# Kernel tuning notes

Hardware: AMD Instinct MI355X
Metric: run time of the kernel (lower is better)

## Reference

```python
import jax, jax.numpy as jnp
import numpy as np

N, L, E, H = 8, 2048, 1024, 1024
EPS = 1e-5


def layernorm(x, g, b):
    m = jnp.mean(x, axis=-1, keepdims=True)
    v = jnp.var(x, axis=-1, keepdims=True)
    return (x - m) * jax.lax.rsqrt(v + EPS) * g + b


def setup_inputs() -> dict:
    key = jax.random.key(0)
    ks = jax.random.split(key, 6)
    s = 0.02
    return {
        "X": jax.random.normal(ks[0], (N, L, E), dtype=jnp.float32),
        "Wq": jax.random.normal(ks[1], (E, H), dtype=jnp.float32) * s,
        "bq": jnp.zeros((H,), jnp.float32),
        "Wk": jax.random.normal(ks[2], (E, H), dtype=jnp.float32) * s,
        "bk": jnp.zeros((H,), jnp.float32),
        "Wv": jax.random.normal(ks[3], (E, H), dtype=jnp.float32) * s,
        "bv": jnp.zeros((H,), jnp.float32),
        "Wf": jax.random.normal(ks[4], (H, H), dtype=jnp.float32) * s,
        "bf": jnp.zeros((H,), jnp.float32),
        "g1": jnp.ones((H,), jnp.float32),
        "b1": jnp.zeros((H,), jnp.float32),
        "g2": jnp.ones((H,), jnp.float32),
        "b2": jnp.zeros((H,), jnp.float32),
    }


def reference(X, Wq, bq, Wk, bk, Wv, bv, Wf, bf, g1, b1, g2, b2):
    scale = 1.0 / jnp.sqrt(jnp.float32(H))
    # both Q and K scaled by 1/sqrt(H) as in source (effective 1/H)
    Q = (X @ Wq + bq) * scale          # (N, L, H)
    K = (X @ Wk + bk) * scale          # (N, L, H)
    V = X @ Wv + bv                    # (N, L, H)
    A = jnp.einsum('nah,nbh->nab', Q, K)   # (N, Lq, Lk)
    A = jax.nn.softmax(A, axis=1)           # softmax over QUERY axis (dim=1), as in source
    # einsum('nll,nlh->nlh') = diagonal of A scaling V elementwise
    diag = jnp.diagonal(A, axis1=1, axis2=2)  # (N, L)
    O = diag[..., None] * V                   # (N, L, H)
    h = layernorm(O + X, g1, b1)
    h = layernorm(h @ Wf + bf + h, g2, b2)
    return h
```

## Files before the change

### kernel.cpp

```cpp
#include <hip/hip_runtime.h>
#include <math.h>

#define NB   8
#define LLEN 2048
#define HDIM 1024
#define LNEPS 1e-5f

#define BM 256
#define BN 256
#define BK 64
#define NT_K (HDIM / BK)
#define NT_K8 (HDIM / 128)
#define NTHR 512
#define SLOT (BM * BK)
#define SLOT8 32768

typedef __attribute__((ext_vector_type(8))) short short8;
typedef __attribute__((ext_vector_type(4))) unsigned short ushort4v;
typedef __attribute__((ext_vector_type(4))) float f32x4;
typedef __attribute__((ext_vector_type(4))) int int4v;
typedef __attribute__((ext_vector_type(8))) int int8v;
typedef __attribute__((ext_vector_type(8))) unsigned char uchar8;

typedef __attribute__((address_space(3))) void lds_void;
typedef const __attribute__((address_space(1))) void glob_void;

__device__ __forceinline__ unsigned short f2bf(float f) {
    union { float f; unsigned u; } v; v.f = f;
    unsigned r = v.u + 0x7FFFu + ((v.u >> 16) & 1u);
    return (unsigned short)(r >> 16);
}
__device__ __forceinline__ float bf2f(unsigned short h) {
    union { unsigned u; float f; } v; v.u = ((unsigned)h) << 16;
    return v.f;
}

__device__ __forceinline__ unsigned char f2fp8(float x) {
    union { float f; unsigned u; } v; v.f = x;
    unsigned s = (v.u >> 24) & 0x80u;
    float a = fabsf(x);
    if (!(a < 448.f)) return (unsigned char)(s | 0x7E);
    int e = (int)((v.u >> 23) & 0xFF) - 127;
    if (e < -6) e = -6;
    float q = rintf(ldexpf(a, 3 - e));
    if (q >= 16.f) { q *= 0.5f; e += 1; }
    int qi = (int)q;
    unsigned byte = (qi < 8) ? (unsigned)qi
                             : (((unsigned)(e + 7) << 3) | (unsigned)(qi - 8));
    return (unsigned char)(s | byte);
}
__device__ __forceinline__ float fp8d(unsigned char b) {
    int e = (b >> 3) & 15, m = b & 7;
    float v = e ? ldexpf((float)(8 + m), e - 10) : ldexpf((float)m, -9);
    return (b & 0x80) ? -v : v;
}

__device__ __forceinline__ unsigned pack4_fp8(float a, float b, float c, float d) {
#if __has_builtin(__builtin_amdgcn_cvt_pk_fp8_f32)
    int r = __builtin_amdgcn_cvt_pk_fp8_f32(a, b, 0, false);
    r = __builtin_amdgcn_cvt_pk_fp8_f32(c, d, r, true);
    return (unsigned)r;
#else
    return (unsigned)f2fp8(a) | ((unsigned)f2fp8(b) << 8)
         | ((unsigned)f2fp8(c) << 16) | ((unsigned)f2fp8(d) << 24);
#endif
}

__device__ __forceinline__ void wg_barrier() {
    asm volatile("" ::: "memory");
    __builtin_amdgcn_s_barrier();
    asm volatile("" ::: "memory");
}

__device__ __forceinline__ void stage_tile(
    const unsigned short* __restrict__ src, int R0, int kcol0,
    unsigned short* ldsDst, int w, int lane)
{
    const int rsub = lane >> 3;
    const int csw  = 8 * ((lane & 7) ^ rsub);
    #pragma unroll
    for (int s = 0; s < 4; ++s) {
        const int r = (s*8 + w)*8 + rsub;
        const unsigned short* g = src + (size_t)(R0 + r) * HDIM + kcol0 + csw;
        __builtin_amdgcn_global_load_lds(
            (glob_void*)g, (lds_void*)(ldsDst + (s*8 + w)*512), 16, 0, 0);
    }
}

__device__ __forceinline__ void run_pipeline(
    const unsigned short* __restrict__ srcA,
    const unsigned short* __restrict__ srcB,
    int rowBase, int colBase, int k0, int nt,
    unsigned short* lds, f32x4 (&acc)[8][4])
{
    const int t = threadIdx.x, w = t >> 6, l = t & 63;
    const int wr = w >> 2, wc = w & 3;
    const int lr = l & 15;
    const int sw = (l & 7) << 4;
    const int aRB = (wr*128 + lr) * 128;
    const int bRB = (wc*64  + lr) * 128;
    const int c0 = ((l >> 4) * 16) ^ sw;
    const int c1 = (64 + ((l >> 4) * 16)) ^ sw;

    unsigned short* sA[2] = { lds,            lds + 2*SLOT };
    unsigned short* sB[2] = { lds + SLOT,     lds + 3*SLOT };

    stage_tile(srcA, rowBase, k0,      sA[0], w, l);
    stage_tile(srcB, colBase, k0,      sB[0], w, l);
    stage_tile(srcA, rowBase, k0 + BK, sA[1], w, l);
    stage_tile(srcB, colBase, k0 + BK, sB[1], w, l);
    asm volatile("s_waitcnt vmcnt(8)" ::: "memory");
    wg_barrier();

    for (int kt = 0; kt < nt; ++kt) {
        const char* bufA = (const char*)sA[kt & 1];
        const char* bufB = (const char*)sB[kt & 1];
        #pragma unroll
        for (int kk = 0; kk < 2; ++kk) {
            const int cc = kk ? c1 : c0;
            short8 af[8], bfr[4];
            #pragma unroll
            for (int mi = 0; mi < 8; ++mi)
                af[mi] = *(const short8*)(bufA + aRB + mi*2048 + cc);
            #pragma unroll
            for (int ni = 0; ni < 4; ++ni)
                bfr[ni] = *(const short8*)(bufB + bRB + ni*2048 + cc);
            #pragma unroll
            for (int mi = 0; mi < 8; ++mi)
                #pragma unroll
                for (int ni = 0; ni < 4; ++ni)
                    acc[mi][ni] = __builtin_amdgcn_mfma_f32_16x16x32_bf16(
                        af[mi], bfr[ni], acc[mi][ni], 0, 0, 0);
        }
        if (kt == nt - 1) break;
        wg_barrier();
        if (kt + 2 < nt) {
            stage_tile(srcA, rowBase, k0 + (kt+2)*BK, sA[kt&1], w, l);
            stage_tile(srcB, colBase, k0 + (kt+2)*BK, sB[kt&1], w, l);
            asm volatile("s_waitcnt vmcnt(8)" ::: "memory");
        } else {
            asm volatile("s_waitcnt vmcnt(0)" ::: "memory");
        }
        wg_barrier();
    }
}

__device__ __forceinline__ void stage_tile8(
    const unsigned char* __restrict__ src, int R0, int kcol0,
    unsigned char* ldsDst, int w, int lane)
{
    const int rsub = lane >> 3;
    const int csw  = ((lane & 7) ^ rsub) << 4;
    #pragma unroll
    for (int s = 0; s < 4; ++s) {
        const int r = (s*8 + w)*8 + rsub;
        __builtin_amdgcn_global_load_lds(
            (glob_void*)(src + (size_t)(R0 + r) * HDIM + kcol0 + csw),
            (lds_void*)(ldsDst + (s*8 + w)*1024), 16, 0, 0);
    }
}

__device__ __forceinline__ void run_pipeline_fp8(
    const unsigned char* __restrict__ srcA,
    const unsigned char* __restrict__ srcB,
    int rowBase, int colBase,
    unsigned char* lds, f32x4 (&acc)[8][4],
    unsigned sa, unsigned sb)
{
    const int t = threadIdx.x, w = t >> 6, l = t & 63;
    const int wr = w >> 2, wc = w & 3;
    const int lr = l & 15;
    const int sw = (l & 7) << 4;
    const int aRB = (wr*128 + lr) * 128;
    const int bRB = (wc*64  + lr) * 128;
    const int g0 = (l >> 4) * 32;
    const int cc0 = g0 ^ sw;
    const int cc1 = (g0 + 16) ^ sw;

    unsigned char* sA[2] = { lds,             lds + 2*SLOT8 };
    unsigned char* sB[2] = { lds + SLOT8,     lds + 3*SLOT8 };

    stage_tile8(srcA, rowBase, 0,   sA[0], w, l);
    stage_tile8(srcB, colBase, 0,   sB[0], w, l);
    stage_tile8(srcA, rowBase, 128, sA[1], w, l);
    stage_tile8(srcB, colBase, 128, sB[1], w, l);
    asm volatile("s_waitcnt vmcnt(8)" ::: "memory");
    wg_barrier();

    for (int kt = 0; kt < NT_K8; ++kt) {
        const char* bufA = (const char*)sA[kt & 1];
        const char* bufB = (const char*)sB[kt & 1];
        int8v b8[4];
        #pragma unroll
        for (int ni = 0; ni < 4; ++ni)
            b8[ni] = __builtin_shufflevector(
                *(const int4v*)(bufB + bRB + ni*2048 + cc0),
                *(const int4v*)(bufB + bRB + ni*2048 + cc1),
                0, 1, 2, 3, 4, 5, 6, 7);
        #pragma unroll
        for (int mi = 0; mi < 8; ++mi) {
            int8v a8 = __builtin_shufflevector(
                *(const int4v*)(bufA + aRB + mi*2048 + cc0),
                *(const int4v*)(bufA + aRB + mi*2048 + cc1),
                0, 1, 2, 3, 4, 5, 6, 7);
            #pragma unroll
            for (int ni = 0; ni < 4; ++ni)
                acc[mi][ni] = __builtin_amdgcn_mfma_scale_f32_16x16x128_f8f6f4(
                    a8, b8[ni], acc[mi][ni], 0, 0, 0, sa, 0, sb);
        }
        if (kt == NT_K8 - 1) break;
        wg_barrier();
        if (kt + 2 < NT_K8) {
            stage_tile8(srcA, rowBase, (kt+2)*128, sA[kt&1], w, l);
            stage_tile8(srcB, colBase, (kt+2)*128, sB[kt&1], w, l);
            asm volatile("s_waitcnt vmcnt(8)" ::: "memory");
        } else {
            asm volatile("s_waitcnt vmcnt(0)" ::: "memory");
        }
        wg_barrier();
    }
}

__global__ __launch_bounds__(NTHR, 2) void gemm_proj(
    const unsigned short* __restrict__ A,
    const unsigned short* __restrict__ Bt,
    const float* __restrict__ bias,
    unsigned short* __restrict__ C,
    float alpha, int gx)
{
    __shared__ __align__(16) unsigned short lds[4 * SLOT];
    const int nwg = gridDim.x, bid = blockIdx.x;
    const int swz = (bid & 7) * (nwg >> 3) + (bid >> 3);
    const int bx = swz % gx, by = swz / gx;
    const int rowBase = by * BM, colBase = bx * BN;

    f32x4 acc[8][4] = {};
    run_pipeline(A, Bt, rowBase, colBase, 0, NT_K, lds, acc);

    const int t = threadIdx.x, w = t >> 6, l = t & 63;
    const int wr = w >> 2, wc = w & 3;
    const int lr = l & 15;

    #pragma unroll
    for (int ni = 0; ni < 4; ++ni) {
        const int col = colBase + wc*64 + ni*16 + lr;
        const float bv = bias[col];
        #pragma unroll
        for (int mi = 0; mi < 8; ++mi) {
            const int row0 = rowBase + wr*128 + mi*16 + (l >> 4) * 4;
            #pragma unroll
            for (int j = 0; j < 4; ++j)
                C[(size_t)(row0 + j) * HDIM + col] = f2bf(alpha * (acc[mi][ni][j] + bv));
        }
    }
}

__global__ __launch_bounds__(NTHR, 2) void gemm_wqk_splitk(
    const unsigned short* __restrict__ Wkb,
    const unsigned short* __restrict__ Wqb,
    float* __restrict__ slabs)
{
    __shared__ __align__(16) unsigned short lds[4 * SLOT];
    const int bid = blockIdx.x;
    const int kz = bid & 3, tile = bid >> 2;
    const int rowBase = (tile >> 2) * BM, colBase = (tile & 3) * BN;

    f32x4 acc[8][4] = {};
    run_pipeline(Wkb, Wqb, rowBase, colBase, kz * (HDIM/4), NT_K/4, lds, acc);

    float* out = slabs + (size_t)kz * HDIM * HDIM;
    const int t = threadIdx.x, w = t >> 6, l = t & 63;
    const int wr = w >> 2, wc = w & 3;
    const int lr = l & 15;

    #pragma unroll
    for (int ni = 0; ni < 4; ++ni) {
        const int col = colBase + wc*64 + ni*16 + lr;
        #pragma unroll
        for (int mi = 0; mi < 8; ++mi) {
            const int row0 = rowBase + wr*128 + mi*16 + (l >> 4) * 4;
            #pragma unroll
            for (int j = 0; j < 4; ++j)
                out[(size_t)(row0 + j) * HDIM + col] = acc[mi][ni][j];
        }
    }
}

__global__ __launch_bounds__(256) void wqk_reduce_cast(
    const float* __restrict__ slabs, unsigned char* __restrict__ out8)
{
    const size_t WEl = (size_t)HDIM * HDIM;
    const size_t i = ((size_t)blockIdx.x * 256 + threadIdx.x) * 4;
    float4 a = *reinterpret_cast<const float4*>(slabs + i);
    float4 b = *reinterpret_cast<const float4*>(slabs + WEl + i);
    float4 c = *reinterpret_cast<const float4*>(slabs + 2*WEl + i);
    float4 d = *reinterpret_cast<const float4*>(slabs + 3*WEl + i);
    unsigned wd = pack4_fp8(64.f*(a.x+b.x+c.x+d.x), 64.f*(a.y+b.y+c.y+d.y),
                            64.f*(a.z+b.z+c.z+d.z), 64.f*(a.w+b.w+c.w+d.w));
    *reinterpret_cast<unsigned*>(out8 + i) = wd;
}

__global__ __launch_bounds__(NTHR, 2) void gemm_proj_fp8(
    const unsigned char* __restrict__ A,
    const unsigned char* __restrict__ Bt,
    const float* __restrict__ bias0, const float* __restrict__ bias1,
    unsigned char* __restrict__ C0, unsigned char* __restrict__ C1,
    float al0, float al1, unsigned sb0, unsigned sb1, int gx)
{
    __shared__ __align__(16) unsigned char lds8[4 * SLOT8];
    const int nwg = gridDim.x, bid = blockIdx.x;
    const int swz = (bid & 7) * (nwg >> 3) + (bid >> 3);
    const int bx = swz % gx, by = swz / gx;
    const int rowBase = by * BM, colBase = bx * BN;

    const int mat = colBase >> 10;

    f32x4 acc[8][4] = {};
    run_pipeline_fp8(A, Bt, rowBase, colBase, lds8, acc,
                     0x7F7F7F7Fu, mat ? sb1 : sb0);

    const int t = threadIdx.x, w = t >> 6, l = t & 63;
    const int wr = w >> 2, wc = w & 3;
    const int lr = l & 15;

    unsigned char* Cm  = mat ? C1 : C0;
    const float* bm    = mat ? bias1 : bias0;
    const float am     = mat ? al1 : al0;
    const int lcb = colBase & (HDIM - 1);

    #pragma unroll
    for (int ni = 0; ni < 4; ++ni) {
        const int col = lcb + wc*64 + ni*16 + lr;
        const float bv = bm[col];
        #pragma unroll
        for (int mi = 0; mi < 8; ++mi) {
            const int row0 = rowBase + wr*128 + mi*16 + (l >> 4) * 4;
            const unsigned wd = pack4_fp8(
                am * (acc[mi][ni][0] + bv), am * (acc[mi][ni][1] + bv),
                am * (acc[mi][ni][2] + bv), am * (acc[mi][ni][3] + bv));
            #pragma unroll
            for (int j = 0; j < 4; ++j)
                Cm[(size_t)(row0 + j) * HDIM + col] = (unsigned char)(wd >> (8*j));
        }
    }
}

__global__ __launch_bounds__(NTHR, 2) void qk_colsum_diag_fp8(
    const unsigned char* __restrict__ Xq8,
    const unsigned char* __restrict__ Xb8,
    const float* __restrict__ uvec,
    float* __restrict__ colsum, float* __restrict__ diagv)
{
    __shared__ __align__(16) unsigned char lds8[4 * SLOT8];
    const int bid = blockIdx.x;
    const int n = bid & 7;
    const int rem = bid >> 3;
    const int rowBase = (rem & 7) * BM;
    const int colBase = (rem >> 3) * BN;
    const unsigned char* An = Xq8 + (size_t)n * LLEN * HDIM;
    const unsigned char* Bn = Xb8 + (size_t)n * LLEN * HDIM;

    f32x4 acc[8][4] = {};
    run_pipeline_fp8(An, Bn, rowBase, colBase, lds8, acc,
                     0x75757575u, 0x7F7F7F7Fu);

    const int t = threadIdx.x, w = t >> 6, l = t & 63;
    const int wr = w >> 2, wc = w & 3;
    const int lr = l & 15;

    float ur[8][4];
    #pragma unroll
    for (int mi = 0; mi < 8; ++mi)
        #pragma unroll
        for (int j = 0; j < 4; ++j)
            ur[mi][j] = uvec[(size_t)n * LLEN + rowBase + wr*128 + mi*16 + (l>>4)*4 + j];

    #pragma unroll
    for (int ni = 0; ni < 4; ++ni) {
        float s = 0.f;
        #pragma unroll
        for (int mi = 0; mi < 8; ++mi)
            #pragma unroll
            for (int j = 0; j < 4; ++j)
                s += __expf(acc[mi][ni][j] + ur[mi][j]);
        s += __shfl_xor(s, 16);
        s += __shfl_xor(s, 32);
        if (l < 16)
            atomicAdd(&colsum[(size_t)n * LLEN + colBase + wc*64 + ni*16 + l], s);
    }

    if (rowBase == colBase && (wc >> 1) == wr) {
        #pragma unroll
        for (int mi = 0; mi < 8; ++mi)
            #pragma unroll
            for (int ni = 0; ni < 4; ++ni)
                #pragma unroll
                for (int j = 0; j < 4; ++j) {
                    const int rr = wr*128 + mi*16 + (l >> 4)*4 + j;
                    const int cc = wc*64 + ni*16 + lr;
                    if (rr == cc)
                        diagv[(size_t)n * LLEN + rowBase + rr] = acc[mi][ni][j];
                }
    }
}

__global__ __launch_bounds__(256) void cast_x_dual(
    const float* __restrict__ in, unsigned short* __restrict__ outb,
    unsigned char* __restrict__ out8, int n8)
{
    int i = blockIdx.x * 256 + threadIdx.x;
    if (i >= n8) return;
    const float4* p = reinterpret_cast<const float4*>(in) + (size_t)i * 2;
    float4 a = p[0], b = p[1];
    short8 o;
    o[0] = (short)f2bf(a.x); o[1] = (short)f2bf(a.y);
    o[2] = (short)f2bf(a.z); o[3] = (short)f2bf(a.w);
    o[4] = (short)f2bf(b.x); o[5] = (short)f2bf(b.y);
    o[6] = (short)f2bf(b.z); o[7] = (short)f2bf(b.w);
    unsigned w0 = pack4_fp8(a.x, a.y, a.z, a.w);
    unsigned w1 = pack4_fp8(b.x, b.y, b.z, b.w);
    *(reinterpret_cast<short8*>(outb) + i) = o;
    uint2 pk; pk.x = w0; pk.y = w1;
    *(reinterpret_cast<uint2*>(out8) + i) = pk;
}

__global__ __launch_bounds__(256) void cast_w2(
    const float* __restrict__ W0, const float* __restrict__ W1,
    unsigned short* __restrict__ out0, unsigned short* __restrict__ out1, int n8)
{
    int i = blockIdx.x * 256 + threadIdx.x;
    if (i >= n8) return;
    const float* in = blockIdx.y ? W1 : W0;
    unsigned short* outp = blockIdx.y ? out1 : out0;
    const float4* p = reinterpret_cast<const float4*>(in) + (size_t)i * 2;
    float4 a = p[0], b = p[1];
    short8 o;
    o[0] = (short)f2bf(a.x); o[1] = (short)f2bf(a.y);
    o[2] = (short)f2bf(a.z); o[3] = (short)f2bf(a.w);
    o[4] = (short)f2bf(b.x); o[5] = (short)f2bf(b.y);
    o[6] = (short)f2bf(b.z); o[7] = (short)f2bf(b.w);
    *(reinterpret_cast<short8*>(outp) + i) = o;
}

__global__ __launch_bounds__(256) void transpose_cast_bf16(
    const float* __restrict__ W, unsigned short* __restrict__ Wt)
{
    __shared__ float tile[32][33];
    const int tx = threadIdx.x & 31, ty = threadIdx.x >> 5;
    const int c0 = blockIdx.x * 32, r0 = blockIdx.y * 32;
    #pragma unroll
    for (int r = 0; r < 4; ++r)
        tile[ty + r*8][tx] = W[(size_t)(r0 + ty + r*8) * HDIM + c0 + tx];
    __syncthreads();
    #pragma unroll
    for (int r = 0; r < 4; ++r)
        Wt[(size_t)(c0 + ty + r*8) * HDIM + r0 + tx] = f2bf(tile[tx][ty + r*8]);
}

__global__ __launch_bounds__(256) void transpose_cast_fp8(
    const float* __restrict__ W, unsigned char* __restrict__ Wt, float scale)
{
    __shared__ float tile[32][33];
    const int tx = threadIdx.x & 31, ty = threadIdx.x >> 5;
    const int c0 = blockIdx.x * 32, r0 = blockIdx.y * 32;
    #pragma unroll
    for (int r = 0; r < 4; ++r)
        tile[ty + r*8][tx] = W[(size_t)(r0 + ty + r*8) * HDIM + c0 + tx];
    __syncthreads();
    #pragma unroll
    for (int r = 0; r < 4; ++r)
        Wt[(size_t)(c0 + ty + r*8) * HDIM + r0 + tx] = f2fp8(tile[tx][ty + r*8] * scale);
}

__global__ __launch_bounds__(256) void pvec_kernel(
    const float* __restrict__ Wq, const float* __restrict__ bk,
    float* __restrict__ p)
{
    const int row = blockIdx.x * 4 + (threadIdx.x >> 6);
    const int l = threadIdx.x & 63;
    float s = 0.f;
    #pragma unroll
    for (int c = 0; c < HDIM; c += 64)
        s += Wq[(size_t)row * HDIM + c + l] * bk[c + l];
    #pragma unroll
    for (int off = 32; off > 0; off >>= 1) s += __shfl_down(s, off);
    if (l == 0) p[row] = s;
}

__global__ __launch_bounds__(256) void uvec_kernel(
    const unsigned short* __restrict__ Xb, const float* __restrict__ p,
    float* __restrict__ u, float sc2)
{
    const int row = blockIdx.x * 4 + (threadIdx.x >> 6);
    const int l = threadIdx.x & 63;
    const unsigned short* xr = Xb + (size_t)row * HDIM + l * 16;
    float s = 0.f;
    #pragma unroll
    for (int k = 0; k < 2; ++k) {
        short8 v = *reinterpret_cast<const short8*>(xr + k*8);
        #pragma unroll
        for (int j = 0; j < 8; ++j)
            s += bf2f((unsigned short)v[j]) * p[l*16 + k*8 + j];
    }
    #pragma unroll
    for (int off = 32; off > 0; off >>= 1) s += __shfl_down(s, off);
    if (l == 0) u[row] = s * sc2;
}

__global__ __launch_bounds__(256) void ln1_kernel(
    const unsigned char* __restrict__ V8, const unsigned short* __restrict__ Xbp,
    const float* __restrict__ colsum, const float* __restrict__ diagval,
    const float* __restrict__ uvec,
    const float* __restrict__ g1, const float* __restrict__ b1,
    unsigned short* __restrict__ h1)
{
    const int row = blockIdx.x;
    const size_t base = (size_t)row * HDIM;
    const float dv = __expf(diagval[row] + uvec[row]) / colsum[row];
    const int h0 = threadIdx.x * 4;

    unsigned vv = *reinterpret_cast<const unsigned*>(&V8[base + h0]);
    ushort4v xx = *reinterpret_cast<const ushort4v*>(&Xbp[base + h0]);
    float y[4];
    y[0] = dv * fp8d((unsigned char)(vv      )) + bf2f(xx[0]);
    y[1] = dv * fp8d((unsigned char)(vv >>  8)) + bf2f(xx[1]);
    y[2] = dv * fp8d((unsigned char)(vv >> 16)) + bf2f(xx[2]);
    y[3] = dv * fp8d((unsigned char)(vv >> 24)) + bf2f(xx[3]);

    float s = y[0]+y[1]+y[2]+y[3];
    float s2 = y[0]*y[0]+y[1]*y[1]+y[2]*y[2]+y[3]*y[3];
    #pragma unroll
    for (int off = 32; off > 0; off >>= 1) {
        s  += __shfl_down(s,  off);
        s2 += __shfl_down(s2, off);
    }
    __shared__ float ws1[4], ws2[4];
    const int wid = threadIdx.x >> 6;
    if ((threadIdx.x & 63) == 0) { ws1[wid] = s; ws2[wid] = s2; }
    __syncthreads();
    const float S  = ws1[0]+ws1[1]+ws1[2]+ws1[3];
    const float S2 = ws2[0]+ws2[1]+ws2[2]+ws2[3];
    const float m   = S  * (1.0f / HDIM);
    const float var = S2 * (1.0f / HDIM) - m*m;
    const float inv = rsqrtf(var + LNEPS);

    float4 gg = *reinterpret_cast<const float4*>(&g1[h0]);
    float4 bb = *reinterpret_cast<const float4*>(&b1[h0]);
    ushort4v o;
    o[0] = f2bf((y[0]-m)*inv*gg.x + bb.x);
    o[1] = f2bf((y[1]-m)*inv*gg.y + bb.y);
    o[2] = f2bf((y[2]-m)*inv*gg.z + bb.z);
    o[3] = f2bf((y[3]-m)*inv*gg.w + bb.w);
    *reinterpret_cast<ushort4v*>(&h1[base + h0]) = o;
}

__global__ __launch_bounds__(256) void ln2_kernel(
    const unsigned short* __restrict__ Gb, const unsigned short* __restrict__ h1b,
    const float* __restrict__ g2, const float* __restrict__ b2,
    float* __restrict__ out)
{
    const int row = blockIdx.x;
    const size_t base = (size_t)row * HDIM;
    const int h0 = threadIdx.x * 4;

    ushort4v gv = *reinterpret_cast<const ushort4v*>(&Gb[base + h0]);
    ushort4v hv = *reinterpret_cast<const ushort4v*>(&h1b[base + h0]);
    float y[4];
    y[0] = bf2f(gv[0]) + bf2f(hv[0]); y[1] = bf2f(gv[1]) + bf2f(hv[1]);
    y[2] = bf2f(gv[2]) + bf2f(hv[2]); y[3] = bf2f(gv[3]) + bf2f(hv[3]);

    float s = y[0]+y[1]+y[2]+y[3];
    float s2 = y[0]*y[0]+y[1]*y[1]+y[2]*y[2]+y[3]*y[3];
    #pragma unroll
    for (int off = 32; off > 0; off >>= 1) {
        s  += __shfl_down(s,  off);
        s2 += __shfl_down(s2, off);
    }
    __shared__ float ws1[4], ws2[4];
    const int wid = threadIdx.x >> 6;
    if ((threadIdx.x & 63) == 0) { ws1[wid] = s; ws2[wid] = s2; }
    __syncthreads();
    const float S  = ws1[0]+ws1[1]+ws1[2]+ws1[3];
    const float S2 = ws2[0]+ws2[1]+ws2[2]+ws2[3];
    const float m   = S  * (1.0f / HDIM);
    const float var = S2 * (1.0f / HDIM) - m*m;
    const float inv = rsqrtf(var + LNEPS);

    float4 gg = *reinterpret_cast<const float4*>(&g2[h0]);
    float4 bb = *reinterpret_cast<const float4*>(&b2[h0]);
    float4 o;
    o.x = (y[0]-m)*inv*gg.x + bb.x;
    o.y = (y[1]-m)*inv*gg.y + bb.y;
    o.z = (y[2]-m)*inv*gg.z + bb.z;
    o.w = (y[3]-m)*inv*gg.w + bb.w;
    *reinterpret_cast<float4*>(&out[base + h0]) = o;
}

extern "C" void kernel_launch(void* const* d_in, const int* in_sizes, int n_in,
                              void* d_out, int out_size, void* d_ws, size_t ws_size,
                              hipStream_t stream) {
    (void)in_sizes; (void)n_in; (void)out_size; (void)ws_size;
    const float* X  = (const float*)d_in[0];
    const float* Wq = (const float*)d_in[1];
    const float* bq = (const float*)d_in[2];   (void)bq;
    const float* Wk = (const float*)d_in[3];
    const float* bk = (const float*)d_in[4];
    const float* Wv = (const float*)d_in[5];
    const float* bv = (const float*)d_in[6];
    const float* Wf = (const float*)d_in[7];
    const float* bf = (const float*)d_in[8];
    const float* g1 = (const float*)d_in[9];
    const float* b1 = (const float*)d_in[10];
    const float* g2 = (const float*)d_in[11];
    const float* b2 = (const float*)d_in[12];
    float* out = (float*)d_out;

    const size_t MATE = (size_t)NB * LLEN * HDIM;
    const size_t WE   = (size_t)HDIM * HDIM;

    unsigned short* Xb  = (unsigned short*)d_out;
    unsigned char*  V8  = (unsigned char*)(Xb + MATE);

    unsigned short* h1b   = (unsigned short*)d_ws;
    unsigned short* Gb    = h1b + MATE;
    unsigned short* WfT   = Gb + MATE;
    unsigned short* Wqb   = WfT + WE;
    unsigned short* Wkb   = Wqb + WE;
    unsigned char*  Wqk8T = (unsigned char*)(Wkb + WE);
    unsigned char*  Wv8T  = Wqk8T + WE;
    float* colsum = (float*)(Wv8T + WE);
    float* diagv  = colsum + (size_t)NB * LLEN;
    float* pv     = diagv + (size_t)NB * LLEN;
    float* uv     = pv + HDIM;
    float* zvec   = uv + (size_t)NB * LLEN;
    unsigned char* Xq8 = (unsigned char*)(zvec + HDIM);
    unsigned char* Xb8 = Xq8 + MATE;
    float* wqkSlabs = (float*)(Xb8 + MATE);

    const int M = NB * LLEN;
    const float sc2 = 1.0f / 1024.0f;

    const size_t mset = (3*(size_t)NB*LLEN + 2*HDIM) * sizeof(float);
    hipMemsetAsync(colsum, 0, mset, stream);

    cast_x_dual<<<(int)(MATE/8) / 256, 256, 0, stream>>>(X, Xb, Xb8, (int)(MATE/8));
    {
        dim3 cg((int)(WE/8) / 256, 2);
        cast_w2<<<cg, 256, 0, stream>>>(Wq, Wk, Wqb, Wkb, (int)(WE/8));
    }
    {
        dim3 tgrid(HDIM / 32, HDIM / 32);
        transpose_cast_bf16<<<tgrid, 256, 0, stream>>>(Wf, WfT);
        transpose_cast_fp8<<<tgrid, 256, 0, stream>>>(Wv, Wv8T, 16.0f);
    }

    gemm_wqk_splitk<<<64, NTHR, 0, stream>>>(Wkb, Wqb, wqkSlabs);
    wqk_reduce_cast<<<(int)(WE/4) / 256, 256, 0, stream>>>(wqkSlabs, Wqk8T);

    pvec_kernel<<<HDIM / 4, 256, 0, stream>>>(Wq, bk, pv);
    uvec_kernel<<<M / 4, 256, 0, stream>>>(Xb, pv, uv, sc2);

    {
        const int gx = 2 * HDIM / BN;
        const int nwg = gx * (M / BM);
        gemm_proj_fp8<<<nwg, NTHR, 0, stream>>>(Xb8, Wqk8T, zvec, bv,
                                                Xq8, V8, 1024.0f, 1.0f,
                                                0x6F6F6F6Fu ,
                                                0x7B7B7B7Bu , gx);
    }

    qk_colsum_diag_fp8<<<512, NTHR, 0, stream>>>(Xq8, Xb8, uv, colsum, diagv);

    ln1_kernel<<<M, 256, 0, stream>>>(V8, Xb, colsum, diagv, uv, g1, b1, h1b);

    {
        const int gx = HDIM / BN;
        const int nwg = gx * (M / BM);
        gemm_proj<<<nwg, NTHR, 0, stream>>>(h1b, WfT, bf, Gb, 1.0f, gx);
    }

    ln2_kernel<<<M, 256, 0, stream>>>(Gb, h1b, g2, b2, out);
}
```

Before: 232.6 us.

## Shrink GEMM tiles to 128x128 with 4-wave workgroups across all matmul kernels

Replaces the 256x256 tile, 8-wave GEMM pipelines with 128x128 tiles using 4 waves (each wave still computes 64x64) for the bf16 and fp8 paths. Grid sizes grow fourfold, e.g. the QK colsum kernel goes from 512 to 2048 workgroups. The aim is better CU occupancy and load balance on a GPU with many CUs. In exchange, arithmetic intensity per tile drops, so more global/L2 traffic is needed and more atomics go to colsum.

```diff
diff --git a/kernel.cpp b/kernel.cpp
--- a/kernel.cpp
+++ b/kernel.cpp
@@ -6,14 +6,12 @@
 #define HDIM 1024
 #define LNEPS 1e-5f
 
-#define BM 256
-#define BN 256
+#define BM 128
 #define BK 64
 #define NT_K (HDIM / BK)
 #define NT_K8 (HDIM / 128)
-#define NTHR 512
-#define SLOT (BM * BK)
-#define SLOT8 32768
+#define NTHR 256
+#define TB 16384
 
 typedef __attribute__((ext_vector_type(8))) short short8;
 typedef __attribute__((ext_vector_type(4))) unsigned short ushort4v;
@@ -72,43 +70,58 @@
     asm volatile("" ::: "memory");
 }
 
-__device__ __forceinline__ void stage_tile(
+__device__ __forceinline__ void stage128_bf16(
     const unsigned short* __restrict__ src, int R0, int kcol0,
-    unsigned short* ldsDst, int w, int lane)
-{
-    const int rsub = lane >> 3;
-    const int csw  = 8 * ((lane & 7) ^ rsub);
+    unsigned short* ldsDst, int w, int l)
+{
+    const int rsub = l >> 3;
+    const int ce = 8 * ((l & 7) ^ rsub);
     #pragma unroll
     for (int s = 0; s < 4; ++s) {
-        const int r = (s*8 + w)*8 + rsub;
-        const unsigned short* g = src + (size_t)(R0 + r) * HDIM + kcol0 + csw;
+        const int r = s*32 + w*8 + rsub;
         __builtin_amdgcn_global_load_lds(
-            (glob_void*)g, (lds_void*)(ldsDst + (s*8 + w)*512), 16, 0, 0);
-    }
-}
-
-__device__ __forceinline__ void run_pipeline(
+            (glob_void*)(src + (size_t)(R0 + r) * HDIM + kcol0 + ce),
+            (lds_void*)(ldsDst + s*2048 + w*512), 16, 0, 0);
+    }
+}
+
+__device__ __forceinline__ void stage128_fp8(
+    const unsigned char* __restrict__ src, int R0, int kcol0,
+    unsigned char* ldsDst, int w, int l)
+{
+    const int rsub = l >> 3;
+    const int cb = ((l & 7) ^ rsub) << 4;
+    #pragma unroll
+    for (int s = 0; s < 4; ++s) {
+        const int r = s*32 + w*8 + rsub;
+        __builtin_amdgcn_global_load_lds(
+            (glob_void*)(src + (size_t)(R0 + r) * HDIM + kcol0 + cb),
+            (lds_void*)(ldsDst + s*4096 + w*1024), 16, 0, 0);
+    }
+}
+
+__device__ __forceinline__ void pipe128_bf16(
     const unsigned short* __restrict__ srcA,
     const unsigned short* __restrict__ srcB,
     int rowBase, int colBase, int k0, int nt,
-    unsigned short* lds, f32x4 (&acc)[8][4])
+    unsigned short* lds, f32x4 (&acc)[4][4])
 {
     const int t = threadIdx.x, w = t >> 6, l = t & 63;
-    const int wr = w >> 2, wc = w & 3;
+    const int wr = w >> 1, wc = w & 1;
     const int lr = l & 15;
     const int sw = (l & 7) << 4;
-    const int aRB = (wr*128 + lr) * 128;
-    const int bRB = (wc*64  + lr) * 128;
+    const int aRB = (wr*64 + lr) * 128;
+    const int bRB = (wc*64 + lr) * 128;
     const int c0 = ((l >> 4) * 16) ^ sw;
     const int c1 = (64 + ((l >> 4) * 16)) ^ sw;
 
-    unsigned short* sA[2] = { lds,            lds + 2*SLOT };
-    unsigned short* sB[2] = { lds + SLOT,     lds + 3*SLOT };
-
-    stage_tile(srcA, rowBase, k0,      sA[0], w, l);
-    stage_tile(srcB, colBase, k0,      sB[0], w, l);
-    stage_tile(srcA, rowBase, k0 + BK, sA[1], w, l);
-    stage_tile(srcB, colBase, k0 + BK, sB[1], w, l);
+    unsigned short* sA[2] = { lds,          lds + 2*(TB/2) };
+    unsigned short* sB[2] = { lds + TB/2,   lds + 3*(TB/2) };
+
+    stage128_bf16(srcA, rowBase, k0,      sA[0], w, l);
+    stage128_bf16(srcB, colBase, k0,      sB[0], w, l);
+    stage128_bf16(srcA, rowBase, k0 + BK, sA[1], w, l);
+    stage128_bf16(srcB, colBase, k0 + BK, sB[1], w, l);
     asm volatile("s_waitcnt vmcnt(8)" ::: "memory");
     wg_barrier();
 
@@ -118,15 +131,15 @@
         #pragma unroll
         for (int kk = 0; kk < 2; ++kk) {
             const int cc = kk ? c1 : c0;
-            short8 af[8], bfr[4];
-            #pragma unroll
-            for (int mi = 0; mi < 8; ++mi)
+            short8 af[4], bfr[4];
+            #pragma unroll
+            for (int mi = 0; mi < 4; ++mi)
                 af[mi] = *(const short8*)(bufA + aRB + mi*2048 + cc);
             #pragma unroll
             for (int ni = 0; ni < 4; ++ni)
                 bfr[ni] = *(const short8*)(bufB + bRB + ni*2048 + cc);
             #pragma unroll
-            for (int mi = 0; mi < 8; ++mi)
+            for (int mi = 0; mi < 4; ++mi)
                 #pragma unroll
                 for (int ni = 0; ni < 4; ++ni)
                     acc[mi][ni] = __builtin_amdgcn_mfma_f32_16x16x32_bf16(
@@ -135,8 +148,8 @@
         if (kt == nt - 1) break;
         wg_barrier();
         if (kt + 2 < nt) {
-            stage_tile(srcA, rowBase, k0 + (kt+2)*BK, sA[kt&1], w, l);
-            stage_tile(srcB, colBase, k0 + (kt+2)*BK, sB[kt&1], w, l);
+            stage128_bf16(srcA, rowBase, k0 + (kt+2)*BK, sA[kt&1], w, l);
+            stage128_bf16(srcB, colBase, k0 + (kt+2)*BK, sB[kt&1], w, l);
             asm volatile("s_waitcnt vmcnt(8)" ::: "memory");
         } else {
             asm volatile("s_waitcnt vmcnt(0)" ::: "memory");
@@ -145,45 +158,30 @@
     }
 }
 
-__device__ __forceinline__ void stage_tile8(
-    const unsigned char* __restrict__ src, int R0, int kcol0,
-    unsigned char* ldsDst, int w, int lane)
-{
-    const int rsub = lane >> 3;
-    const int csw  = ((lane & 7) ^ rsub) << 4;
-    #pragma unroll
-    for (int s = 0; s < 4; ++s) {
-        const int r = (s*8 + w)*8 + rsub;
-        __builtin_amdgcn_global_load_lds(
-            (glob_void*)(src + (size_t)(R0 + r) * HDIM + kcol0 + csw),
-            (lds_void*)(ldsDst + (s*8 + w)*1024), 16, 0, 0);
-    }
-}
-
-__device__ __forceinline__ void run_pipeline_fp8(
+__device__ __forceinline__ void pipe128_fp8(
     const unsigned char* __restrict__ srcA,
     const unsigned char* __restrict__ srcB,
     int rowBase, int colBase,
-    unsigned char* lds, f32x4 (&acc)[8][4],
+    unsigned char* lds, f32x4 (&acc)[4][4],
     unsigned sa, unsigned sb)
 {
     const int t = threadIdx.x, w = t >> 6, l = t & 63;
-    const int wr = w >> 2, wc = w & 3;
+    const int wr = w >> 1, wc = w & 1;
     const int lr = l & 15;
     const int sw = (l & 7) << 4;
-    const int aRB = (wr*128 + lr) * 128;
-    const int bRB = (wc*64  + lr) * 128;
+    const int aRB = (wr*64 + lr) * 128;
+    const int bRB = (wc*64 + lr) * 128;
     const int g0 = (l >> 4) * 32;
     const int cc0 = g0 ^ sw;
     const int cc1 = (g0 + 16) ^ sw;
 
-    unsigned char* sA[2] = { lds,             lds + 2*SLOT8 };
-    unsigned char* sB[2] = { lds + SLOT8,     lds + 3*SLOT8 };
-
-    stage_tile8(srcA, rowBase, 0,   sA[0], w, l);
-    stage_tile8(srcB, colBase, 0,   sB[0], w, l);
-    stage_tile8(srcA, rowBase, 128, sA[1], w, l);
-    stage_tile8(srcB, colBase, 128, sB[1], w, l);
+    unsigned char* sA[2] = { lds,        lds + 2*TB };
+    unsigned char* sB[2] = { lds + TB,   lds + 3*TB };
+
+    stage128_fp8(srcA, rowBase, 0,   sA[0], w, l);
+    stage128_fp8(srcB, colBase, 0,   sB[0], w, l);
+    stage128_fp8(srcA, rowBase, 128, sA[1], w, l);
+    stage128_fp8(srcB, colBase, 128, sB[1], w, l);
     asm volatile("s_waitcnt vmcnt(8)" ::: "memory");
     wg_barrier();
 
@@ -198,7 +196,7 @@
                 *(const int4v*)(bufB + bRB + ni*2048 + cc1),
                 0, 1, 2, 3, 4, 5, 6, 7);
         #pragma unroll
-        for (int mi = 0; mi < 8; ++mi) {
+        for (int mi = 0; mi < 4; ++mi) {
             int8v a8 = __builtin_shufflevector(
                 *(const int4v*)(bufA + aRB + mi*2048 + cc0),
                 *(const int4v*)(bufA + aRB + mi*2048 + cc1),
@@ -211,8 +209,8 @@
         if (kt == NT_K8 - 1) break;
         wg_barrier();
         if (kt + 2 < NT_K8) {
-            stage_tile8(srcA, rowBase, (kt+2)*128, sA[kt&1], w, l);
-            stage_tile8(srcB, colBase, (kt+2)*128, sB[kt&1], w, l);
+            stage128_fp8(srcA, rowBase, (kt+2)*128, sA[kt&1], w, l);
+            stage128_fp8(srcB, colBase, (kt+2)*128, sB[kt&1], w, l);
             asm volatile("s_waitcnt vmcnt(8)" ::: "memory");
         } else {
             asm volatile("s_waitcnt vmcnt(0)" ::: "memory");
@@ -221,24 +219,24 @@
     }
 }
 
-__global__ __launch_bounds__(NTHR, 2) void gemm_proj(
+__global__ __launch_bounds__(NTHR) void gemm_proj(
     const unsigned short* __restrict__ A,
     const unsigned short* __restrict__ Bt,
     const float* __restrict__ bias,
     unsigned short* __restrict__ C,
     float alpha, int gx)
 {
-    __shared__ __align__(16) unsigned short lds[4 * SLOT];
+    __shared__ __align__(16) unsigned short lds[2 * TB];
     const int nwg = gridDim.x, bid = blockIdx.x;
     const int swz = (bid & 7) * (nwg >> 3) + (bid >> 3);
     const int bx = swz % gx, by = swz / gx;
-    const int rowBase = by * BM, colBase = bx * BN;
-
-    f32x4 acc[8][4] = {};
-    run_pipeline(A, Bt, rowBase, colBase, 0, NT_K, lds, acc);
+    const int rowBase = by * BM, colBase = bx * BM;
+
+    f32x4 acc[4][4] = {};
+    pipe128_bf16(A, Bt, rowBase, colBase, 0, NT_K, lds, acc);
 
     const int t = threadIdx.x, w = t >> 6, l = t & 63;
-    const int wr = w >> 2, wc = w & 3;
+    const int wr = w >> 1, wc = w & 1;
     const int lr = l & 15;
 
     #pragma unroll
@@ -246,8 +244,8 @@
         const int col = colBase + wc*64 + ni*16 + lr;
         const float bv = bias[col];
         #pragma unroll
-        for (int mi = 0; mi < 8; ++mi) {
-            const int row0 = rowBase + wr*128 + mi*16 + (l >> 4) * 4;
+        for (int mi = 0; mi < 4; ++mi) {
+            const int row0 = rowBase + wr*64 + mi*16 + (l >> 4) * 4;
             #pragma unroll
             for (int j = 0; j < 4; ++j)
                 C[(size_t)(row0 + j) * HDIM + col] = f2bf(alpha * (acc[mi][ni][j] + bv));
@@ -255,30 +253,30 @@
     }
 }
 
-__global__ __launch_bounds__(NTHR, 2) void gemm_wqk_splitk(
+__global__ __launch_bounds__(NTHR) void gemm_wqk_splitk(
     const unsigned short* __restrict__ Wkb,
     const unsigned short* __restrict__ Wqb,
     float* __restrict__ slabs)
 {
-    __shared__ __align__(16) unsigned short lds[4 * SLOT];
+    __shared__ __align__(16) unsigned short lds[2 * TB];
     const int bid = blockIdx.x;
     const int kz = bid & 3, tile = bid >> 2;
-    const int rowBase = (tile >> 2) * BM, colBase = (tile & 3) * BN;
-
-    f32x4 acc[8][4] = {};
-    run_pipeline(Wkb, Wqb, rowBase, colBase, kz * (HDIM/4), NT_K/4, lds, acc);
+    const int rowBase = (tile >> 3) * BM, colBase = (tile & 7) * BM;
+
+    f32x4 acc[4][4] = {};
+    pipe128_bf16(Wkb, Wqb, rowBase, colBase, kz * (HDIM/4), NT_K/4, lds, acc);
 
     float* out = slabs + (size_t)kz * HDIM * HDIM;
     const int t = threadIdx.x, w = t >> 6, l = t & 63;
-    const int wr = w >> 2, wc = w & 3;
+    const int wr = w >> 1, wc = w & 1;
     const int lr = l & 15;
 
     #pragma unroll
     for (int ni = 0; ni < 4; ++ni) {
         const int col = colBase + wc*64 + ni*16 + lr;
         #pragma unroll
-        for (int mi = 0; mi < 8; ++mi) {
-            const int row0 = rowBase + wr*128 + mi*16 + (l >> 4) * 4;
+        for (int mi = 0; mi < 4; ++mi) {
+            const int row0 = rowBase + wr*64 + mi*16 + (l >> 4) * 4;
             #pragma unroll
             for (int j = 0; j < 4; ++j)
                 out[(size_t)(row0 + j) * HDIM + col] = acc[mi][ni][j];
@@ -300,27 +298,27 @@
     *reinterpret_cast<unsigned*>(out8 + i) = wd;
 }
 
-__global__ __launch_bounds__(NTHR, 2) void gemm_proj_fp8(
+__global__ __launch_bounds__(NTHR) void gemm_proj_fp8(
     const unsigned char* __restrict__ A,
     const unsigned char* __restrict__ Bt,
     const float* __restrict__ bias0, const float* __restrict__ bias1,
     unsigned char* __restrict__ C0, unsigned char* __restrict__ C1,
     float al0, float al1, unsigned sb0, unsigned sb1, int gx)
 {
-    __shared__ __align__(16) unsigned char lds8[4 * SLOT8];
+    __shared__ __align__(16) unsigned char lds8[4 * TB];
     const int nwg = gridDim.x, bid = blockIdx.x;
     const int swz = (bid & 7) * (nwg >> 3) + (bid >> 3);
     const int bx = swz % gx, by = swz / gx;
-    const int rowBase = by * BM, colBase = bx * BN;
+    const int rowBase = by * BM, colBase = bx * BM;
 
     const int mat = colBase >> 10;
 
-    f32x4 acc[8][4] = {};
-    run_pipeline_fp8(A, Bt, rowBase, colBase, lds8, acc,
-                     0x7F7F7F7Fu, mat ? sb1 : sb0);
+    f32x4 acc[4][4] = {};
+    pipe128_fp8(A, Bt, rowBase, colBase, lds8, acc,
+                0x7F7F7F7Fu, mat ? sb1 : sb0);
 
     const int t = threadIdx.x, w = t >> 6, l = t & 63;
-    const int wr = w >> 2, wc = w & 3;
+    const int wr = w >> 1, wc = w & 1;
     const int lr = l & 15;
 
     unsigned char* Cm  = mat ? C1 : C0;
@@ -333,8 +331,8 @@
         const int col = lcb + wc*64 + ni*16 + lr;
         const float bv = bm[col];
         #pragma unroll
-        for (int mi = 0; mi < 8; ++mi) {
-            const int row0 = rowBase + wr*128 + mi*16 + (l >> 4) * 4;
+        for (int mi = 0; mi < 4; ++mi) {
+            const int row0 = rowBase + wr*64 + mi*16 + (l >> 4) * 4;
             const unsigned wd = pack4_fp8(
                 am * (acc[mi][ni][0] + bv), am * (acc[mi][ni][1] + bv),
                 am * (acc[mi][ni][2] + bv), am * (acc[mi][ni][3] + bv));
@@ -345,41 +343,41 @@
     }
 }
 
-__global__ __launch_bounds__(NTHR, 2) void qk_colsum_diag_fp8(
+__global__ __launch_bounds__(NTHR) void qk_colsum_diag_fp8(
     const unsigned char* __restrict__ Xq8,
     const unsigned char* __restrict__ Xb8,
     const float* __restrict__ uvec,
     float* __restrict__ colsum, float* __restrict__ diagv)
 {
-    __shared__ __align__(16) unsigned char lds8[4 * SLOT8];
+    __shared__ __align__(16) unsigned char lds8[4 * TB];
     const int bid = blockIdx.x;
     const int n = bid & 7;
     const int rem = bid >> 3;
-    const int rowBase = (rem & 7) * BM;
-    const int colBase = (rem >> 3) * BN;
+    const int rowBase = (rem & 15) * BM;
+    const int colBase = (rem >> 4) * BM;
     const unsigned char* An = Xq8 + (size_t)n * LLEN * HDIM;
     const unsigned char* Bn = Xb8 + (size_t)n * LLEN * HDIM;
 
-    f32x4 acc[8][4] = {};
-    run_pipeline_fp8(An, Bn, rowBase, colBase, lds8, acc,
-                     0x75757575u, 0x7F7F7F7Fu);
+    f32x4 acc[4][4] = {};
+    pipe128_fp8(An, Bn, rowBase, colBase, lds8, acc,
+                0x75757575u, 0x7F7F7F7Fu);
 
     const int t = threadIdx.x, w = t >> 6, l = t & 63;
-    const int wr = w >> 2, wc = w & 3;
+    const int wr = w >> 1, wc = w & 1;
     const int lr = l & 15;
 
-    float ur[8][4];
-    #pragma unroll
-    for (int mi = 0; mi < 8; ++mi)
+    float ur[4][4];
+    #pragma unroll
+    for (int mi = 0; mi < 4; ++mi)
         #pragma unroll
         for (int j = 0; j < 4; ++j)
-            ur[mi][j] = uvec[(size_t)n * LLEN + rowBase + wr*128 + mi*16 + (l>>4)*4 + j];
+            ur[mi][j] = uvec[(size_t)n * LLEN + rowBase + wr*64 + mi*16 + (l>>4)*4 + j];
 
     #pragma unroll
     for (int ni = 0; ni < 4; ++ni) {
         float s = 0.f;
         #pragma unroll
-        for (int mi = 0; mi < 8; ++mi)
+        for (int mi = 0; mi < 4; ++mi)
             #pragma unroll
             for (int j = 0; j < 4; ++j)
                 s += __expf(acc[mi][ni][j] + ur[mi][j]);
@@ -389,14 +387,14 @@
             atomicAdd(&colsum[(size_t)n * LLEN + colBase + wc*64 + ni*16 + l], s);
     }
 
-    if (rowBase == colBase && (wc >> 1) == wr) {
-        #pragma unroll
-        for (int mi = 0; mi < 8; ++mi)
+    if (rowBase == colBase && wr == wc) {
+        #pragma unroll
+        for (int mi = 0; mi < 4; ++mi)
             #pragma unroll
             for (int ni = 0; ni < 4; ++ni)
                 #pragma unroll
                 for (int j = 0; j < 4; ++j) {
-                    const int rr = wr*128 + mi*16 + (l >> 4)*4 + j;
+                    const int rr = wr*64 + mi*16 + (l >> 4)*4 + j;
                     const int cc = wc*64 + ni*16 + lr;
                     if (rr == cc)
                         diagv[(size_t)n * LLEN + rowBase + rr] = acc[mi][ni][j];
@@ -654,14 +652,14 @@
         transpose_cast_fp8<<<tgrid, 256, 0, stream>>>(Wv, Wv8T, 16.0f);
     }
 
-    gemm_wqk_splitk<<<64, NTHR, 0, stream>>>(Wkb, Wqb, wqkSlabs);
+    gemm_wqk_splitk<<<256, NTHR, 0, stream>>>(Wkb, Wqb, wqkSlabs);
     wqk_reduce_cast<<<(int)(WE/4) / 256, 256, 0, stream>>>(wqkSlabs, Wqk8T);
 
     pvec_kernel<<<HDIM / 4, 256, 0, stream>>>(Wq, bk, pv);
     uvec_kernel<<<M / 4, 256, 0, stream>>>(Xb, pv, uv, sc2);
 
     {
-        const int gx = 2 * HDIM / BN;
+        const int gx = 2 * HDIM / BM;
         const int nwg = gx * (M / BM);
         gemm_proj_fp8<<<nwg, NTHR, 0, stream>>>(Xb8, Wqk8T, zvec, bv,
                                                 Xq8, V8, 1024.0f, 1.0f,
@@ -669,12 +667,12 @@
                                                 0x7B7B7B7Bu , gx);
     }
 
-    qk_colsum_diag_fp8<<<512, NTHR, 0, stream>>>(Xq8, Xb8, uv, colsum, diagv);
+    qk_colsum_diag_fp8<<<2048, NTHR, 0, stream>>>(Xq8, Xb8, uv, colsum, diagv);
 
     ln1_kernel<<<M, 256, 0, stream>>>(V8, Xb, colsum, diagv, uv, g1, b1, h1b);
 
     {
-        const int gx = HDIM / BN;
+        const int gx = HDIM / BM;
         const int nwg = gx * (M / BM);
         gemm_proj<<<nwg, NTHR, 0, stream>>>(h1b, WfT, bf, Gb, 1.0f, gx);
     }
```

Measured after the change: 228.5 us. About the same (-1.8%).
